# Kernel optimization log

Measured on AMD Instinct MI355X. Metric: run time of the kernel, lower is better.

The kernel has to match this reference:

```python
import jax, jax.numpy as jnp
import numpy as np

TAU = 0.5          # critic_fract
RA = 0.5           # risk_aversion (reg_trad)
EPS = 1e-4         # combined_pdf + 0.0001 passed as sqrt_prob_weights^2
N_LOC = 101
SUPPORT = jnp.linspace(0.0, 1.0, N_LOC)  # support grid, ascending


def _mlp_softmax(x, W1, b1, W2, b2, W3, b3):
    h = jax.nn.relu(x @ W1 + b1)
    h = jax.nn.relu(h @ W2 + b2)
    return jax.nn.softmax(h @ W3 + b3, axis=-1)  # [B, E] combination weights


def _solve_newsvendor(p):
    """Exact solution of the cvxpy QP per sample:
       min_z>=0  2(1-RA) * sum_i p_i * max(TAU*e_i, (TAU-1)*e_i)
                 + 2*RA * sum_i q_i * e_i^2,   e_i = s_i - z,  q_i = p_i + EPS.
    Convex piecewise-quadratic in scalar z -> enumerate the stationary point of
    each inter-kink interval, clip to the interval, take the argmin.
    """
    q = p + EPS                                  # [B, n]
    Q = q.sum(-1, keepdims=True)                 # [B, 1]
    Sq = (q * SUPPORT).sum(-1, keepdims=True)    # [B, 1]
    P = p.sum(-1, keepdims=True)                 # [B, 1]
    # C[:, k] = mass strictly below z when z lies in interval k
    C = jnp.concatenate([jnp.zeros_like(p[:, :1]), jnp.cumsum(p, axis=-1)], axis=-1)  # [B, n+1]
    # stationary point of the quadratic+linear objective on interval k
    z_unc = (Sq + (1.0 - RA) * (TAU * (P - C) - (1.0 - TAU) * C) / (2.0 * RA)) / Q    # [B, n+1]
    lower = jnp.concatenate([jnp.zeros((1,), SUPPORT.dtype), SUPPORT])   # [n+1]
    upper = jnp.concatenate([SUPPORT, SUPPORT[-1:]])                      # [n+1]
    cand = jnp.clip(z_unc, lower[None, :], upper[None, :])                # [B, n+1]
    # evaluate objective at all candidates:  e [B, K, n]
    e = SUPPORT[None, None, :] - cand[:, :, None]
    pin = jnp.maximum(TAU * e, (TAU - 1.0) * e)
    obj = (2.0 * (1.0 - RA)) * jnp.einsum('bn,bkn->bk', p, pin) \
        + (2.0 * RA) * jnp.einsum('bn,bkn->bk', q, e * e)
    k = jax.lax.stop_gradient(jnp.argmin(obj, axis=-1))                   # [B]
    z = jnp.take_along_axis(cand, k[:, None], axis=-1)                    # [B, 1]
    error = SUPPORT[None, :] - z                                          # [B, n]
    return z, error


def setup_inputs() -> dict:
    key = jax.random.key(0)
    ks = jax.random.split(key, 16)
    B, D, H, E = 4096, 64, 128, 8
    x = jax.random.normal(ks[0], (B, D), jnp.float32)
    inp = {'x': x}
    for i in range(E):
        p = jax.random.uniform(ks[1 + i], (B, N_LOC), jnp.float32)
        inp[f'p{i}'] = p / p.sum(-1, keepdims=True)  # probability vectors
    inp['W1'] = jax.random.normal(ks[9], (D, H), jnp.float32) / np.sqrt(D)
    inp['b1'] = jnp.zeros((H,), jnp.float32)
    inp['W2'] = jax.random.normal(ks[10], (H, H), jnp.float32) / np.sqrt(H)
    inp['b2'] = jnp.zeros((H,), jnp.float32)
    inp['W3'] = jax.random.normal(ks[11], (H, E), jnp.float32) / np.sqrt(H)
    inp['b3'] = jnp.zeros((E,), jnp.float32)
    return inp


def reference(x, p0, p1, p2, p3, p4, p5, p6, p7, W1, b1, W2, b2, W3, b3):
    w = _mlp_softmax(x, W1, b1, W2, b2, W3, b3)          # [B, E]
    Pexp = jnp.stack([p0, p1, p2, p3, p4, p5, p6, p7], axis=1)  # [B, E, n]
    combined_pdf = jnp.einsum('be,ben->bn', w, Pexp)     # convex combination
    z, error = _solve_newsvendor(combined_pdf)
    return (combined_pdf, z, error)
```

## Files before the change

### kernel.cpp

```cpp
#include <hip/hip_runtime.h>
#include <hip/hip_bf16.h>
#include <float.h>

#define N_LOC 101
#define TAUC 0.5f
#define RAC  0.5f
#define EPSV 1e-4f

__device__ __forceinline__ float wsum64(float v) {
    #pragma unroll
    for (int off = 32; off; off >>= 1) v += __shfl_xor(v, off);
    return v;
}

__device__ __forceinline__ void fma4(float* acc, float s, float4 v) {
    acc[0] += s * v.x; acc[1] += s * v.y;
    acc[2] += s * v.z; acc[3] += s * v.w;
}

__global__ __launch_bounds__(256, 2) void fused8_kernel(
    const float* __restrict__ x,
    const float* __restrict__ p0, const float* __restrict__ p1,
    const float* __restrict__ p2, const float* __restrict__ p3,
    const float* __restrict__ p4, const float* __restrict__ p5,
    const float* __restrict__ p6, const float* __restrict__ p7,
    const float* __restrict__ W1, const float* __restrict__ b1,
    const float* __restrict__ W2, const float* __restrict__ b2,
    const float* __restrict__ W3, const float* __restrict__ b3,
    float* __restrict__ out_pdf, float* __restrict__ out_z,
    float* __restrict__ out_err, int B)
{
    __shared__ float xs [8 * 64];
    __shared__ float hp [8][8 * 128];
    __shared__ float h1s[8 * 128];
    __shared__ float h2s[8 * 128];

    const int t   = threadIdx.x;
    const int r0b = blockIdx.x * 8;

    if (t < 128)
        *reinterpret_cast<float4*>(&xs[t * 4]) =
            *reinterpret_cast<const float4*>(&x[r0b * 64 + t * 4]);
    __syncthreads();

    const int jg = t & 31;
    const int j0 = jg * 4;
    const int kh = t >> 5;

    {
        float acc[8][4] = {};
        const int kb = kh * 8;
        #pragma unroll
        for (int kq = 0; kq < 8; kq += 4) {
            float4 w[4];
            #pragma unroll
            for (int q = 0; q < 4; ++q)
                w[q] = *reinterpret_cast<const float4*>(&W1[(kb + kq + q) * 128 + j0]);
            #pragma unroll
            for (int r = 0; r < 8; ++r) {
                const float4 xv = *reinterpret_cast<const float4*>(&xs[r * 64 + kb + kq]);
                fma4(acc[r], xv.x, w[0]);
                fma4(acc[r], xv.y, w[1]);
                fma4(acc[r], xv.z, w[2]);
                fma4(acc[r], xv.w, w[3]);
            }
        }
        #pragma unroll
        for (int r = 0; r < 8; ++r) {
            float4 o; o.x = acc[r][0]; o.y = acc[r][1]; o.z = acc[r][2]; o.w = acc[r][3];
            *reinterpret_cast<float4*>(&hp[kh][r * 128 + j0]) = o;
        }
    }
    __syncthreads();
    {
        const int r  = t >> 5;
        const int jj = (t & 31) * 4;
        float4 a = *reinterpret_cast<const float4*>(&b1[jj]);
        #pragma unroll
        for (int k2 = 0; k2 < 8; ++k2) {
            const float4 q = *reinterpret_cast<const float4*>(&hp[k2][r * 128 + jj]);
            a.x += q.x; a.y += q.y; a.z += q.z; a.w += q.w;
        }
        float4 o;
        o.x = fmaxf(a.x, 0.f); o.y = fmaxf(a.y, 0.f);
        o.z = fmaxf(a.z, 0.f); o.w = fmaxf(a.w, 0.f);
        *reinterpret_cast<float4*>(&h1s[r * 128 + jj]) = o;
    }
    __syncthreads();

    {
        float acc[8][4] = {};
        const int kb = kh * 16;
        #pragma unroll
        for (int kq = 0; kq < 16; kq += 4) {
            float4 w[4];
            #pragma unroll
            for (int q = 0; q < 4; ++q)
                w[q] = *reinterpret_cast<const float4*>(&W2[(kb + kq + q) * 128 + j0]);
            #pragma unroll
            for (int r = 0; r < 8; ++r) {
                const float4 hv = *reinterpret_cast<const float4*>(&h1s[r * 128 + kb + kq]);
                fma4(acc[r], hv.x, w[0]);
                fma4(acc[r], hv.y, w[1]);
                fma4(acc[r], hv.z, w[2]);
                fma4(acc[r], hv.w, w[3]);
            }
        }
        #pragma unroll
        for (int r = 0; r < 8; ++r) {
            float4 o; o.x = acc[r][0]; o.y = acc[r][1]; o.z = acc[r][2]; o.w = acc[r][3];
            *reinterpret_cast<float4*>(&hp[kh][r * 128 + j0]) = o;
        }
    }
    __syncthreads();
    {
        const int r  = t >> 5;
        const int jj = (t & 31) * 4;
        float4 a = *reinterpret_cast<const float4*>(&b2[jj]);
        #pragma unroll
        for (int k2 = 0; k2 < 8; ++k2) {
            const float4 q = *reinterpret_cast<const float4*>(&hp[k2][r * 128 + jj]);
            a.x += q.x; a.y += q.y; a.z += q.z; a.w += q.w;
        }
        float4 o;
        o.x = fmaxf(a.x, 0.f); o.y = fmaxf(a.y, 0.f);
        o.z = fmaxf(a.z, 0.f); o.w = fmaxf(a.w, 0.f);
        *reinterpret_cast<float4*>(&h2s[r * 128 + jj]) = o;
    }
    __syncthreads();

    const int wid  = t >> 6;
    const int lane = t & 63;
    const int e    = lane & 7;
    const int kc   = lane >> 3;
    const int n1 = lane, n2 = lane + 64;
    const bool v2 = (n2 < N_LOC);
    const float s1 = n1 * 0.01f, s2 = n2 * 0.01f;

    for (int rr = 0; rr < 2; ++rr) {
        const int rl  = wid * 2 + rr;
        const int row = r0b + rl;

        float acc3 = 0.f;
        #pragma unroll
        for (int i = 0; i < 16; ++i)
            acc3 += h2s[rl * 128 + kc * 16 + i] * W3[(kc * 16 + i) * 8 + e];
        acc3 += __shfl_xor(acc3, 8);
        acc3 += __shfl_xor(acc3, 16);
        acc3 += __shfl_xor(acc3, 32);
        const float logit = acc3 + b3[e];
        float m = logit;
        m = fmaxf(m, __shfl_xor(m, 1));
        m = fmaxf(m, __shfl_xor(m, 2));
        m = fmaxf(m, __shfl_xor(m, 4));
        const float ex = expf(logit - m);
        float s = ex;
        s += __shfl_xor(s, 1);
        s += __shfl_xor(s, 2);
        s += __shfl_xor(s, 4);
        const float wgt = ex / s;

        float wv8[8];
        #pragma unroll
        for (int e2 = 0; e2 < 8; ++e2) wv8[e2] = __shfl(wgt, e2);

        const long base = (long)row * N_LOC;
        float pdf1, pdf2;
        {
            const float* pp[8] = { p0+base, p1+base, p2+base, p3+base,
                                   p4+base, p5+base, p6+base, p7+base };
            pdf1 = 0.f; pdf2 = 0.f;
            #pragma unroll
            for (int ee = 0; ee < 8; ++ee) {
                pdf1 += wv8[ee] * pp[ee][n1];
                pdf2 += wv8[ee] * (v2 ? pp[ee][n2] : 0.f);
            }
        }
        out_pdf[base + n1] = pdf1;
        if (v2) out_pdf[base + n2] = pdf2;

        const float P   = wsum64(pdf1 + pdf2);
        const float Sp  = wsum64(pdf1*s1  + pdf2*s2);
        const float Sp2 = wsum64(pdf1*s1*s1 + pdf2*s2*s2);
        const float Q   = P   + (float)N_LOC * EPSV;
        const float Sq  = Sp  + 50.5f  * EPSV;
        const float Sq2 = Sp2 + 33.835f * EPSV;

        float ap = pdf1, bp = pdf2, aps = pdf1*s1, bps = pdf2*s2;
        #pragma unroll
        for (int off = 1; off < 64; off <<= 1) {
            float t0 = __shfl_up(ap,  off);
            float t1 = __shfl_up(bp,  off);
            float t2 = __shfl_up(aps, off);
            float t3 = __shfl_up(bps, off);
            if (lane >= off) { ap += t0; bp += t1; aps += t2; bps += t3; }
        }
        const float TaP  = __shfl(ap,  63);
        const float TaPs = __shfl(aps, 63);
        float eC1 = __shfl_up(ap,  1); if (lane == 0) eC1 = 0.f;
        float eB1 = __shfl_up(aps, 1); if (lane == 0) eB1 = 0.f;
        float eC2 = __shfl_up(bp,  1); if (lane == 0) eC2 = 0.f;
        float eB2 = __shfl_up(bps, 1); if (lane == 0) eB2 = 0.f;
        eC2 += TaP; eB2 += TaPs;

        auto evalc = [&](int k, float C, float Bv, float& zout) -> float {
            const float lo = (k == 0)   ? 0.f : (k - 1) * 0.01f;
            const float hi = (k <= 100) ? k * 0.01f : 1.f;
            float zu = (Sq + (1.f - RAC) * (TAUC * (P - C) - (1.f - TAUC) * C)
                              / (2.f * RAC)) / Q;
            float z = fminf(fmaxf(zu, lo), hi);
            float pin  = TAUC * ((Sp - Bv) - z * (P - C)) + (1.f - TAUC) * (z * C - Bv);
            float quad = Sq2 - 2.f * z * Sq + z * z * Q;
            zout = z;
            return 2.f * (1.f - RAC) * pin + 2.f * RAC * quad;
        };
        float z1 = 0.f, z2 = 0.f;
        const float o1 = evalc(n1, eC1, eB1, z1);
        const float o2 = v2 ? evalc(n2, eC2, eB2, z2) : FLT_MAX;

        float bobj; int bk; float bz;
        if (o2 < o1) { bobj = o2; bk = n2; bz = z2; }
        else         { bobj = o1; bk = n1; bz = z1; }
        #pragma unroll
        for (int off = 32; off; off >>= 1) {
            float oo = __shfl_xor(bobj, off);
            int   ok = __shfl_xor(bk,   off);
            float oz = __shfl_xor(bz,   off);
            if (oo < bobj || (oo == bobj && ok < bk)) { bobj = oo; bk = ok; bz = oz; }
        }

        if (lane == 0) out_z[row] = bz;
        out_err[base + n1] = s1 - bz;
        if (v2) out_err[base + n2] = s2 - bz;
    }
}

extern "C" void kernel_launch(void* const* d_in, const int* in_sizes, int n_in,
                              void* d_out, int out_size, void* d_ws, size_t ws_size,
                              hipStream_t stream)
{
    const float* x  = (const float*)d_in[0];
    const float* p[8];
    for (int e = 0; e < 8; ++e) p[e] = (const float*)d_in[1 + e];
    const float* W1 = (const float*)d_in[9];
    const float* b1 = (const float*)d_in[10];
    const float* W2 = (const float*)d_in[11];
    const float* b2 = (const float*)d_in[12];
    const float* W3 = (const float*)d_in[13];
    const float* b3 = (const float*)d_in[14];

    const int B = in_sizes[0] / 64;
    float* out_pdf = (float*)d_out;
    float* out_z   = out_pdf + (size_t)B * N_LOC;
    float* out_err = out_z + B;

    fused8_kernel<<<B / 8, 256, 0, stream>>>(
        x, p[0], p[1], p[2], p[3], p[4], p[5], p[6], p[7],
        W1, b1, W2, b2, W3, b3, out_pdf, out_z, out_err, B);
}
```

Baseline: 15.63 us.

## Prefetch expert pdfs and MLP weights into registers before dependent compute

Moves the global loads of all eight expert probability rows to the very start of the kernel. It also loads the W1, W2 and W3 slices into registers before the barriers that precede their use, so this memory latency overlaps the MLP layers instead of sitting on the critical path. The row loop is unrolled so the prefetched registers can be indexed statically. This raises register pressure (32 pdf values plus 24 float4 weights per thread), which could cause spills or lower occupancy under the 256x2 launch bounds.

```diff
diff --git a/kernel.cpp b/kernel.cpp
--- a/kernel.cpp
+++ b/kernel.cpp
@@ -38,117 +38,149 @@
     const int t   = threadIdx.x;
     const int r0b = blockIdx.x * 8;
 
-    if (t < 128)
-        *reinterpret_cast<float4*>(&xs[t * 4]) =
-            *reinterpret_cast<const float4*>(&x[r0b * 64 + t * 4]);
-    __syncthreads();
-
     const int jg = t & 31;
     const int j0 = jg * 4;
     const int kh = t >> 5;
-
-    {
-        float acc[8][4] = {};
-        const int kb = kh * 8;
-        #pragma unroll
-        for (int kq = 0; kq < 8; kq += 4) {
-            float4 w[4];
-            #pragma unroll
-            for (int q = 0; q < 4; ++q)
-                w[q] = *reinterpret_cast<const float4*>(&W1[(kb + kq + q) * 128 + j0]);
-            #pragma unroll
-            for (int r = 0; r < 8; ++r) {
-                const float4 xv = *reinterpret_cast<const float4*>(&xs[r * 64 + kb + kq]);
-                fma4(acc[r], xv.x, w[0]);
-                fma4(acc[r], xv.y, w[1]);
-                fma4(acc[r], xv.z, w[2]);
-                fma4(acc[r], xv.w, w[3]);
-            }
-        }
-        #pragma unroll
-        for (int r = 0; r < 8; ++r) {
-            float4 o; o.x = acc[r][0]; o.y = acc[r][1]; o.z = acc[r][2]; o.w = acc[r][3];
-            *reinterpret_cast<float4*>(&hp[kh][r * 128 + j0]) = o;
-        }
-    }
-    __syncthreads();
-    {
-        const int r  = t >> 5;
-        const int jj = (t & 31) * 4;
-        float4 a = *reinterpret_cast<const float4*>(&b1[jj]);
-        #pragma unroll
-        for (int k2 = 0; k2 < 8; ++k2) {
-            const float4 q = *reinterpret_cast<const float4*>(&hp[k2][r * 128 + jj]);
-            a.x += q.x; a.y += q.y; a.z += q.z; a.w += q.w;
-        }
-        float4 o;
-        o.x = fmaxf(a.x, 0.f); o.y = fmaxf(a.y, 0.f);
-        o.z = fmaxf(a.z, 0.f); o.w = fmaxf(a.w, 0.f);
-        *reinterpret_cast<float4*>(&h1s[r * 128 + jj]) = o;
-    }
-    __syncthreads();
-
-    {
-        float acc[8][4] = {};
-        const int kb = kh * 16;
-        #pragma unroll
-        for (int kq = 0; kq < 16; kq += 4) {
-            float4 w[4];
-            #pragma unroll
-            for (int q = 0; q < 4; ++q)
-                w[q] = *reinterpret_cast<const float4*>(&W2[(kb + kq + q) * 128 + j0]);
-            #pragma unroll
-            for (int r = 0; r < 8; ++r) {
-                const float4 hv = *reinterpret_cast<const float4*>(&h1s[r * 128 + kb + kq]);
-                fma4(acc[r], hv.x, w[0]);
-                fma4(acc[r], hv.y, w[1]);
-                fma4(acc[r], hv.z, w[2]);
-                fma4(acc[r], hv.w, w[3]);
-            }
-        }
-        #pragma unroll
-        for (int r = 0; r < 8; ++r) {
-            float4 o; o.x = acc[r][0]; o.y = acc[r][1]; o.z = acc[r][2]; o.w = acc[r][3];
-            *reinterpret_cast<float4*>(&hp[kh][r * 128 + j0]) = o;
-        }
-    }
-    __syncthreads();
-    {
-        const int r  = t >> 5;
-        const int jj = (t & 31) * 4;
-        float4 a = *reinterpret_cast<const float4*>(&b2[jj]);
-        #pragma unroll
-        for (int k2 = 0; k2 < 8; ++k2) {
-            const float4 q = *reinterpret_cast<const float4*>(&hp[k2][r * 128 + jj]);
-            a.x += q.x; a.y += q.y; a.z += q.z; a.w += q.w;
-        }
-        float4 o;
-        o.x = fmaxf(a.x, 0.f); o.y = fmaxf(a.y, 0.f);
-        o.z = fmaxf(a.z, 0.f); o.w = fmaxf(a.w, 0.f);
-        *reinterpret_cast<float4*>(&h2s[r * 128 + jj]) = o;
-    }
-    __syncthreads();
-
     const int wid  = t >> 6;
     const int lane = t & 63;
     const int e    = lane & 7;
     const int kc   = lane >> 3;
     const int n1 = lane, n2 = lane + 64;
     const bool v2 = (n2 < N_LOC);
+
+    const int rowA = r0b + wid * 2;
+    const int rowB = rowA + 1;
+    const long baseA = (long)rowA * N_LOC;
+    const long baseB = (long)rowB * N_LOC;
+    float pA[16], pB[16];
+    {
+        const float* pp[8] = { p0, p1, p2, p3, p4, p5, p6, p7 };
+        #pragma unroll
+        for (int ee = 0; ee < 8; ++ee) {
+            pA[ee*2]   = pp[ee][baseA + n1];
+            pA[ee*2+1] = v2 ? pp[ee][baseA + n2] : 0.f;
+            pB[ee*2]   = pp[ee][baseB + n1];
+            pB[ee*2+1] = v2 ? pp[ee][baseB + n2] : 0.f;
+        }
+    }
+
+    float4 w1[8];
+    {
+        const int kb = kh * 8;
+        #pragma unroll
+        for (int kq = 0; kq < 8; ++kq)
+            w1[kq] = *reinterpret_cast<const float4*>(&W1[(kb + kq) * 128 + j0]);
+    }
+
+    if (t < 128)
+        *reinterpret_cast<float4*>(&xs[t * 4]) =
+            *reinterpret_cast<const float4*>(&x[r0b * 64 + t * 4]);
+    __syncthreads();
+
+    {
+        float acc[8][4] = {};
+        const int kb = kh * 8;
+        #pragma unroll
+        for (int kq = 0; kq < 8; kq += 4) {
+            #pragma unroll
+            for (int r = 0; r < 8; ++r) {
+                const float4 xv = *reinterpret_cast<const float4*>(&xs[r * 64 + kb + kq]);
+                fma4(acc[r], xv.x, w1[kq + 0]);
+                fma4(acc[r], xv.y, w1[kq + 1]);
+                fma4(acc[r], xv.z, w1[kq + 2]);
+                fma4(acc[r], xv.w, w1[kq + 3]);
+            }
+        }
+        #pragma unroll
+        for (int r = 0; r < 8; ++r) {
+            float4 o; o.x = acc[r][0]; o.y = acc[r][1]; o.z = acc[r][2]; o.w = acc[r][3];
+            *reinterpret_cast<float4*>(&hp[kh][r * 128 + j0]) = o;
+        }
+    }
+
+    float4 w2[16];
+    {
+        const int kb = kh * 16;
+        #pragma unroll
+        for (int kq = 0; kq < 16; ++kq)
+            w2[kq] = *reinterpret_cast<const float4*>(&W2[(kb + kq) * 128 + j0]);
+    }
+    __syncthreads();
+    {
+        const int r  = t >> 5;
+        const int jj = (t & 31) * 4;
+        float4 a = *reinterpret_cast<const float4*>(&b1[jj]);
+        #pragma unroll
+        for (int k2 = 0; k2 < 8; ++k2) {
+            const float4 q = *reinterpret_cast<const float4*>(&hp[k2][r * 128 + jj]);
+            a.x += q.x; a.y += q.y; a.z += q.z; a.w += q.w;
+        }
+        float4 o;
+        o.x = fmaxf(a.x, 0.f); o.y = fmaxf(a.y, 0.f);
+        o.z = fmaxf(a.z, 0.f); o.w = fmaxf(a.w, 0.f);
+        *reinterpret_cast<float4*>(&h1s[r * 128 + jj]) = o;
+    }
+    __syncthreads();
+
+    {
+        float acc[8][4] = {};
+        const int kb = kh * 16;
+        #pragma unroll
+        for (int kq = 0; kq < 16; kq += 4) {
+            #pragma unroll
+            for (int r = 0; r < 8; ++r) {
+                const float4 hv = *reinterpret_cast<const float4*>(&h1s[r * 128 + kb + kq]);
+                fma4(acc[r], hv.x, w2[kq + 0]);
+                fma4(acc[r], hv.y, w2[kq + 1]);
+                fma4(acc[r], hv.z, w2[kq + 2]);
+                fma4(acc[r], hv.w, w2[kq + 3]);
+            }
+        }
+        #pragma unroll
+        for (int r = 0; r < 8; ++r) {
+            float4 o; o.x = acc[r][0]; o.y = acc[r][1]; o.z = acc[r][2]; o.w = acc[r][3];
+            *reinterpret_cast<float4*>(&hp[kh][r * 128 + j0]) = o;
+        }
+    }
+
+    float w3r[16];
+    #pragma unroll
+    for (int i = 0; i < 16; ++i) w3r[i] = W3[(kc * 16 + i) * 8 + e];
+    const float b3e = b3[e];
+
+    __syncthreads();
+    {
+        const int r  = t >> 5;
+        const int jj = (t & 31) * 4;
+        float4 a = *reinterpret_cast<const float4*>(&b2[jj]);
+        #pragma unroll
+        for (int k2 = 0; k2 < 8; ++k2) {
+            const float4 q = *reinterpret_cast<const float4*>(&hp[k2][r * 128 + jj]);
+            a.x += q.x; a.y += q.y; a.z += q.z; a.w += q.w;
+        }
+        float4 o;
+        o.x = fmaxf(a.x, 0.f); o.y = fmaxf(a.y, 0.f);
+        o.z = fmaxf(a.z, 0.f); o.w = fmaxf(a.w, 0.f);
+        *reinterpret_cast<float4*>(&h2s[r * 128 + jj]) = o;
+    }
+    __syncthreads();
+
     const float s1 = n1 * 0.01f, s2 = n2 * 0.01f;
 
+    #pragma unroll
     for (int rr = 0; rr < 2; ++rr) {
         const int rl  = wid * 2 + rr;
         const int row = r0b + rl;
+        const long base = rr ? baseB : baseA;
 
         float acc3 = 0.f;
         #pragma unroll
         for (int i = 0; i < 16; ++i)
-            acc3 += h2s[rl * 128 + kc * 16 + i] * W3[(kc * 16 + i) * 8 + e];
+            acc3 += h2s[rl * 128 + kc * 16 + i] * w3r[i];
         acc3 += __shfl_xor(acc3, 8);
         acc3 += __shfl_xor(acc3, 16);
         acc3 += __shfl_xor(acc3, 32);
-        const float logit = acc3 + b3[e];
+        const float logit = acc3 + b3e;
         float m = logit;
         m = fmaxf(m, __shfl_xor(m, 1));
         m = fmaxf(m, __shfl_xor(m, 2));
@@ -164,17 +196,13 @@
         #pragma unroll
         for (int e2 = 0; e2 < 8; ++e2) wv8[e2] = __shfl(wgt, e2);
 
-        const long base = (long)row * N_LOC;
-        float pdf1, pdf2;
-        {
-            const float* pp[8] = { p0+base, p1+base, p2+base, p3+base,
-                                   p4+base, p5+base, p6+base, p7+base };
-            pdf1 = 0.f; pdf2 = 0.f;
-            #pragma unroll
-            for (int ee = 0; ee < 8; ++ee) {
-                pdf1 += wv8[ee] * pp[ee][n1];
-                pdf2 += wv8[ee] * (v2 ? pp[ee][n2] : 0.f);
-            }
+        float pdf1 = 0.f, pdf2 = 0.f;
+        #pragma unroll
+        for (int ee = 0; ee < 8; ++ee) {
+            const float a1 = rr ? pB[ee*2]   : pA[ee*2];
+            const float a2 = rr ? pB[ee*2+1] : pA[ee*2+1];
+            pdf1 += wv8[ee] * a1;
+            pdf2 += wv8[ee] * a2;
         }
         out_pdf[base + n1] = pdf1;
         if (v2) out_pdf[base + n2] = pdf2;
```

New measurement: 15.66 us. About the same (+0.2%).

## Replace objective evaluation and argmin reduction with ballot-based interval search

Applied to the files above, without the earlier changes.

Uses the convexity of the piecewise objective: the minimizer lies in the last interval whose unconstrained stationary point is at or above its lower bound. A wave ballot plus count-leading-zeros finds that interval, so the objective no longer has to be evaluated per candidate. This also drops the weighted second-moment reduction, the s-weighted prefix scans and the argmin shuffle reduction. The risk is small differences from the reference in tie and clipping edge cases, and reliance on the monotonicity assumption.

```diff
diff --git a/kernel.cpp b/kernel.cpp
--- a/kernel.cpp
+++ b/kernel.cpp
@@ -179,55 +179,42 @@
         out_pdf[base + n1] = pdf1;
         if (v2) out_pdf[base + n2] = pdf2;
 
-        const float P   = wsum64(pdf1 + pdf2);
-        const float Sp  = wsum64(pdf1*s1  + pdf2*s2);
-        const float Sp2 = wsum64(pdf1*s1*s1 + pdf2*s2*s2);
-        const float Q   = P   + (float)N_LOC * EPSV;
-        const float Sq  = Sp  + 50.5f  * EPSV;
-        const float Sq2 = Sp2 + 33.835f * EPSV;
-
-        float ap = pdf1, bp = pdf2, aps = pdf1*s1, bps = pdf2*s2;
+        float ap = pdf1, bp = pdf2;
         #pragma unroll
         for (int off = 1; off < 64; off <<= 1) {
-            float t0 = __shfl_up(ap,  off);
-            float t1 = __shfl_up(bp,  off);
-            float t2 = __shfl_up(aps, off);
-            float t3 = __shfl_up(bps, off);
-            if (lane >= off) { ap += t0; bp += t1; aps += t2; bps += t3; }
-        }
-        const float TaP  = __shfl(ap,  63);
-        const float TaPs = __shfl(aps, 63);
-        float eC1 = __shfl_up(ap,  1); if (lane == 0) eC1 = 0.f;
-        float eB1 = __shfl_up(aps, 1); if (lane == 0) eB1 = 0.f;
-        float eC2 = __shfl_up(bp,  1); if (lane == 0) eC2 = 0.f;
-        float eB2 = __shfl_up(bps, 1); if (lane == 0) eB2 = 0.f;
-        eC2 += TaP; eB2 += TaPs;
-
-        auto evalc = [&](int k, float C, float Bv, float& zout) -> float {
-            const float lo = (k == 0)   ? 0.f : (k - 1) * 0.01f;
-            const float hi = (k <= 100) ? k * 0.01f : 1.f;
-            float zu = (Sq + (1.f - RAC) * (TAUC * (P - C) - (1.f - TAUC) * C)
-                              / (2.f * RAC)) / Q;
-            float z = fminf(fmaxf(zu, lo), hi);
-            float pin  = TAUC * ((Sp - Bv) - z * (P - C)) + (1.f - TAUC) * (z * C - Bv);
-            float quad = Sq2 - 2.f * z * Sq + z * z * Q;
-            zout = z;
-            return 2.f * (1.f - RAC) * pin + 2.f * RAC * quad;
-        };
-        float z1 = 0.f, z2 = 0.f;
-        const float o1 = evalc(n1, eC1, eB1, z1);
-        const float o2 = v2 ? evalc(n2, eC2, eB2, z2) : FLT_MAX;
-
-        float bobj; int bk; float bz;
-        if (o2 < o1) { bobj = o2; bk = n2; bz = z2; }
-        else         { bobj = o1; bk = n1; bz = z1; }
-        #pragma unroll
-        for (int off = 32; off; off >>= 1) {
-            float oo = __shfl_xor(bobj, off);
-            int   ok = __shfl_xor(bk,   off);
-            float oz = __shfl_xor(bz,   off);
-            if (oo < bobj || (oo == bobj && ok < bk)) { bobj = oo; bk = ok; bz = oz; }
-        }
+            float t0 = __shfl_up(ap, off);
+            float t1 = __shfl_up(bp, off);
+            if (lane >= off) { ap += t0; bp += t1; }
+        }
+        const float TaP = __shfl(ap, 63);
+        const float TbP = __shfl(bp, 63);
+        const float P   = TaP + TbP;
+        const float Sp  = wsum64(pdf1*s1 + pdf2*s2);
+        const float Q   = P  + (float)N_LOC * EPSV;
+        const float Sq  = Sp + 50.5f * EPSV;
+
+        float eC1 = __shfl_up(ap, 1); if (lane == 0) eC1 = 0.f;
+        float eC2 = __shfl_up(bp, 1); if (lane == 0) eC2 = 0.f;
+        eC2 += TaP;
+
+        const float zu1 = (Sq + 0.25f * P - 0.5f * eC1) / Q;
+        const float zu2 = (Sq + 0.25f * P - 0.5f * eC2) / Q;
+        const float lo1 = (n1 == 0) ? 0.f : (n1 - 1) * 0.01f;
+        const float hi1 = n1 * 0.01f;
+        const float lo2 = (n2 - 1) * 0.01f;
+        const float hi2 = n2 * 0.01f;
+
+        const unsigned long long m1 = __ballot(zu1 >= lo1);
+        const unsigned long long m2 = __ballot(v2 && (zu2 >= lo2));
+
+        int kstar;
+        if (m2) kstar = 64 + (63 - __builtin_clzll(m2));
+        else    kstar = 63 - __builtin_clzll(m1);
+
+        const float z1c = fminf(fmaxf(zu1, lo1), hi1);
+        const float z2c = fminf(fmaxf(zu2, lo2), hi2);
+        const int   kl  = (kstar >= 64) ? (kstar - 64) : kstar;
+        const float bz  = __shfl((kstar >= 64) ? z2c : z1c, kl);
 
         if (lane == 0) out_z[row] = bz;
         out_err[base + n1] = s1 - bz;
```

New measurement: 13.86 us. 11.3% less time.
